# Optimization experiments

Hardware: AMD Instinct MI355X
Metric: run time of the kernel (lower is better)

The kernel has to match this reference:

```python
import jax, jax.numpy as jnp
import numpy as np

B, T, I, H = 128, 1024, 512, 1024

def setup_inputs() -> dict:
    key = jax.random.key(0)
    ks = jax.random.split(key, 7)
    stdv = 1.0 / np.sqrt(H)
    u = lambda k, shape: jax.random.uniform(k, shape, jnp.float32, -stdv, stdv)
    return {
        "x": jax.random.normal(ks[0], (B, T, I), jnp.float32),
        "lens": jax.random.randint(ks[1], (B,), 1, T + 1),
        "W": u(ks[2], (I, 4 * H)),
        "U": u(ks[3], (H, 4 * H)),
        "P": u(ks[4], (H, 2 * H)),
        "P_o": u(ks[5], (H, H)),
        "bias": u(ks[6], (4 * H,)),
    }

def reference(x, lens, W, U, P, P_o, bias):
    hs = P_o.shape[0]
    # Precompute input contribution to gates once: [B, T, 4H]
    xW = jnp.einsum('bti,ig->btg', x, W) + bias

    def step(c, g_x):
        gates = g_x + c @ U                      # [B, 4H] (gates use c_t, per source)
        peep = c @ P                             # [B, 2H]
        i_t = jax.nn.sigmoid(gates[:, :hs] + jnp.tanh(peep[:, :hs]))
        f_t = jax.nn.sigmoid(gates[:, hs:2 * hs] + jnp.tanh(peep[:, hs:]))
        g_t = jnp.tanh(gates[:, 2 * hs:3 * hs])
        c_new = f_t * c + i_t * g_t
        o_t = jax.nn.sigmoid(gates[:, 3 * hs:] + jnp.tanh(c_new @ P_o))
        h_t = o_t * jnp.tanh(c_new)
        return c_new, h_t

    c0 = jnp.zeros((x.shape[0], hs), x.dtype)
    _, h_seq = jax.lax.scan(step, c0, jnp.swapaxes(xW, 0, 1))  # h_seq: [T, B, H]
    h_seq = jnp.swapaxes(h_seq, 0, 1)                          # [B, T, H]
    batch_idx = jnp.arange(x.shape[0])
    return h_seq[batch_idx, lens - 1, :]
```

## Files before the change

kernel.cpp:

```cpp
#include <hip/hip_runtime.h>

typedef unsigned short u16;
typedef unsigned long long u64;
typedef __attribute__((ext_vector_type(8))) short bf16x8;
typedef __attribute__((ext_vector_type(4))) float f32x4;
typedef __attribute__((ext_vector_type(4))) u16 u16x4;


__device__ __forceinline__ float bf2f(u16 u) { return __uint_as_float(((unsigned)u) << 16); }
__device__ __forceinline__ u16 f2bf(float f) {
  unsigned u = __float_as_uint(f);
  u = (u + 0x7FFFu + ((u >> 16) & 1u)) >> 16;
  return (u16)u;
}
__device__ __forceinline__ float sigm_(float x) { return 1.0f / (1.0f + __expf(-x)); }
__device__ __forceinline__ float tanh_(float x) {
  float e = __expf(2.0f * fabsf(x));
  float r = 1.0f - 2.0f / (e + 1.0f);
  return copysignf(r, x);
}
__device__ __forceinline__ void g2l16(const void* g, void* l) {
  __builtin_amdgcn_global_load_lds(
      (const __attribute__((address_space(1))) void*)g,
      (__attribute__((address_space(3))) void*)l, 16, 0, 0);
}

__global__ __launch_bounds__(256) void k_cvt(const float* __restrict__ in,
                                             u16* __restrict__ out, int n) {
  int i = (blockIdx.x * 256 + threadIdx.x) * 4;
  if (i >= n) return;
  const float4 v = *(const float4*)(in + i);
  u16x4 o;
  o.x = f2bf(v.x); o.y = f2bf(v.y); o.z = f2bf(v.z); o.w = f2bf(v.w);
  *(u16x4*)(out + i) = o;
}

__global__ __launch_bounds__(256) void k_tr(const float* __restrict__ src, int ld,
                                            u16* __restrict__ out, int K) {
  __shared__ float tle[64][65];
  int j0 = blockIdx.x * 64, k0 = blockIdx.y * 64;
  int jc = threadIdx.x & 63, kq = threadIdx.x >> 6;
  #pragma unroll
  for (int p = 0; p < 16; ++p) {
    int kr = kq * 16 + p;
    tle[jc][kr] = src[(size_t)(k0 + kr) * ld + j0 + jc];
  }
  __syncthreads();
  #pragma unroll
  for (int p = 0; p < 16; ++p) {
    int jr = kq * 16 + p;
    out[(size_t)(j0 + jr) * K + k0 + jc] = f2bf(tle[jr][jc]);
  }
}

__global__ __launch_bounds__(256) void k_gemm(const u16* __restrict__ A,
                                              const u16* __restrict__ Bt,
                                              const float* __restrict__ bias,
                                              u16* __restrict__ xw) {
  __shared__ u16 lds[16384];
  const int Kd = 512;
  int n0 = blockIdx.x * 128, m0 = blockIdx.y * 128;
  int tid = threadIdx.x, lane = tid & 63, wave = tid >> 6;
  int wm = (wave >> 1) * 64, wn = (wave & 1) * 64;
  int l15 = lane & 15, lk8 = (lane >> 4) * 8;
  f32x4 acc[4][4];
  #pragma unroll
  for (int i = 0; i < 4; ++i)
    #pragma unroll
    for (int j = 0; j < 4; ++j) {
      acc[i][j][0] = 0.f; acc[i][j][1] = 0.f; acc[i][j][2] = 0.f; acc[i][j][3] = 0.f;
    }
  for (int k0 = 0; k0 < Kd; k0 += 64) {
    #pragma unroll
    for (int p = 0; p < 8; ++p) {
      int c = p * 256 + tid;
      int ldsbase = (c - lane) * 16;
      int row = (c & 1023) >> 3, colb = (c & 7) * 16;
      const char* g;
      if (c < 1024) g = (const char*)A  + ((size_t)(m0 + row) * Kd + k0) * 2 + colb;
      else          g = (const char*)Bt + ((size_t)(n0 + row) * Kd + k0) * 2 + colb;
      g2l16(g, (char*)lds + ldsbase);
    }
    __syncthreads();
    #pragma unroll
    for (int kk = 0; kk < 2; ++kk) {
      bf16x8 af[4], bfr[4];
      #pragma unroll
      for (int mf = 0; mf < 4; ++mf)
        af[mf] = *(const bf16x8*)&lds[(wm + mf * 16 + l15) * 64 + kk * 32 + lk8];
      #pragma unroll
      for (int nf = 0; nf < 4; ++nf)
        bfr[nf] = *(const bf16x8*)&lds[8192 + (wn + nf * 16 + l15) * 64 + kk * 32 + lk8];
      #pragma unroll
      for (int mf = 0; mf < 4; ++mf)
        #pragma unroll
        for (int nf = 0; nf < 4; ++nf)
          acc[mf][nf] = __builtin_amdgcn_mfma_f32_16x16x32_bf16(af[mf], bfr[nf], acc[mf][nf], 0, 0, 0);
    }
    __syncthreads();
  }
  int rbase = (lane >> 4) * 4;
  #pragma unroll
  for (int mf = 0; mf < 4; ++mf)
    #pragma unroll
    for (int nf = 0; nf < 4; ++nf) {
      int n = n0 + wn + nf * 16 + l15;
      float bv = bias[n];
      int g = n >> 10, j = n & 1023;
      int jbp = j >> 4, col = j & 15;
      #pragma unroll
      for (int r = 0; r < 4; ++r) {
        int m = m0 + wm + mf * 16 + rbase + r;
        int b = m >> 10, t = m & 1023;
        xw[(((size_t)t * 64 + jbp) * 128 + b) * 48 + g * 16 + col] =
            f2bf(acc[mf][nf][r] + bv);
      }
    }
}

__device__ __forceinline__ void gbar_rb(unsigned* bar, unsigned phase, int jb, int rb) {
  __syncthreads();
  if (threadIdx.x == 0) {
    unsigned* barg = bar + rb * 256;
    unsigned* gc = barg + (jb >> 5) * 32;
    unsigned* master = barg + 128;
    unsigned v = __hip_atomic_fetch_add(gc, 1u, __ATOMIC_RELAXED, __HIP_MEMORY_SCOPE_AGENT) + 1;
    if (v == 32u * phase)
      __hip_atomic_fetch_add(master, 1u, __ATOMIC_RELAXED, __HIP_MEMORY_SCOPE_AGENT);
    while (__hip_atomic_load(master, __ATOMIC_RELAXED, __HIP_MEMORY_SCOPE_AGENT) < 2u * phase)
      __builtin_amdgcn_s_sleep(1);
  }
  __syncthreads();
}

__global__ __launch_bounds__(320) void k_persist(
    u16* __restrict__ cb, const u16* __restrict__ wcat, const u16* __restrict__ xw,
    const int* __restrict__ lens, float* __restrict__ sp, float* __restrict__ sn,
    unsigned* __restrict__ bar) {
  __shared__ __align__(16) char smem[98304];
  char* Ab = smem;
  float* sgl = (float*)(smem + 65536);

  const int bid = blockIdx.x;
  const int jb = bid & 63, rb = bid >> 6;
  const int tid = threadIdx.x;
  const int lane = tid & 63, wave = tid >> 6;
  const int l15 = lane & 15, lhi = lane >> 4;
  const int swz = (l15 & 7) << 4;

  const u16* brow = wcat + ((size_t)(wave * 1024 + jb * 16 + l15)) * 1024 + lhi * 8;
  bf16x8 breg[32];
  #pragma unroll
  for (int kf = 0; kf < 32; ++kf)
    breg[kf] = *(const bf16x8*)(brow + kf * 32);

  const int erow = tid >> 3, ejj = (tid & 7) * 2;
  const int eb = rb * 32 + erow;
  const int ej0 = jb * 16 + ejj;
  const int mylen = (tid < 256) ? lens[eb] : 0;
  float c0 = 0.f, c1 = 0.f;

  #pragma unroll 1
  for (int t = 0; t < 1024; ++t) {
    const u64* asrc = (const u64*)((const char*)cb + (size_t)(t & 1) * 262144 +
                                   (size_t)rb * 65536);
    u16* cbout = cb + (size_t)((t + 1) & 1) * 131072;

    unsigned xg0 = 0, xg1 = 0, xg2 = 0;
    if (tid < 256) {
      const u16* xr = xw + (((size_t)t * 64 + jb) * 128 + eb) * 48 + ejj;
      xg0 = *(const unsigned*)(xr);
      xg1 = *(const unsigned*)(xr + 16);
      xg2 = *(const unsigned*)(xr + 32);
    }

    u64 av[26];
    #pragma unroll
    for (int i = 0; i < 26; ++i) {
      int c = i * 320 + tid;
      if (c < 8192)
        av[i] = __hip_atomic_load(asrc + c, __ATOMIC_RELAXED, __HIP_MEMORY_SCOPE_AGENT);
    }
    #pragma unroll
    for (int i = 0; i < 26; ++i) {
      int c = i * 320 + tid;
      if (c < 8192) {
        int row = c >> 8, col8 = c & 255;
        *(u64*)(Ab + row * 2048 + ((col8 * 8) ^ ((row & 7) << 4))) = av[i];
      }
    }
    __syncthreads();

    f32x4 acc0 = {0.f, 0.f, 0.f, 0.f}, acc1 = {0.f, 0.f, 0.f, 0.f};
    f32x4 acc2 = {0.f, 0.f, 0.f, 0.f}, acc3 = {0.f, 0.f, 0.f, 0.f};
    #pragma unroll
    for (int kf = 0; kf < 32; kf += 2) {
      int koffA = (kf * 64 + lhi * 16) ^ swz;
      int koffB = ((kf + 1) * 64 + lhi * 16) ^ swz;
      bf16x8 a0 = *(const bf16x8*)(Ab + l15 * 2048 + koffA);
      bf16x8 a1 = *(const bf16x8*)(Ab + (16 + l15) * 2048 + koffA);
      bf16x8 b0 = *(const bf16x8*)(Ab + l15 * 2048 + koffB);
      bf16x8 b1 = *(const bf16x8*)(Ab + (16 + l15) * 2048 + koffB);
      acc0 = __builtin_amdgcn_mfma_f32_16x16x32_bf16(a0, breg[kf], acc0, 0, 0, 0);
      acc1 = __builtin_amdgcn_mfma_f32_16x16x32_bf16(a1, breg[kf], acc1, 0, 0, 0);
      acc2 = __builtin_amdgcn_mfma_f32_16x16x32_bf16(b0, breg[kf + 1], acc2, 0, 0, 0);
      acc3 = __builtin_amdgcn_mfma_f32_16x16x32_bf16(b1, breg[kf + 1], acc3, 0, 0, 0);
    }
    acc0[0] += acc2[0]; acc0[1] += acc2[1]; acc0[2] += acc2[2]; acc0[3] += acc2[3];
    acc1[0] += acc3[0]; acc1[1] += acc3[1]; acc1[2] += acc3[2]; acc1[3] += acc3[3];

    *(f32x4*)&sgl[(wave * 16 + l15) * 36 + lhi * 4] = acc0;
    *(f32x4*)&sgl[(wave * 16 + l15) * 36 + 16 + lhi * 4] = acc1;
    __syncthreads();

    if (tid < 256) {
      float ci[2] = {c0, c1};
      float cn2[2];
      u16 nb2[2];
      unsigned xg[3] = {xg0, xg1, xg2};
      #pragma unroll
      for (int e = 0; e < 2; ++e) {
        int col = ejj + e;
        float gi = sgl[(0 * 16 + col) * 36 + erow] + bf2f((u16)(xg[0] >> (e * 16)));
        float gf = sgl[(1 * 16 + col) * 36 + erow] + bf2f((u16)(xg[1] >> (e * 16)));
        float gg = sgl[(2 * 16 + col) * 36 + erow] + bf2f((u16)(xg[2] >> (e * 16)));
        float pi = sgl[(3 * 16 + col) * 36 + erow];
        float pf = sgl[(4 * 16 + col) * 36 + erow];
        float it = sigm_(gi + tanh_(pi));
        float ft = sigm_(gf + tanh_(pf));
        float gt = tanh_(gg);
        float cn = ft * ci[e] + it * gt;
        cn2[e] = cn;
        nb2[e] = f2bf(cn);
      }
      c0 = cn2[0]; c1 = cn2[1];
      __hip_atomic_store((unsigned*)(cbout + (size_t)eb * 1024 + ej0),
                         (unsigned)nb2[0] | ((unsigned)nb2[1] << 16),
                         __ATOMIC_RELAXED, __HIP_MEMORY_SCOPE_AGENT);
      if (t == mylen - 1) {
        *(float2*)(sp + (size_t)eb * 1024 + ej0) = make_float2(ci[0], ci[1]);
        *(float2*)(sn + (size_t)eb * 1024 + ej0) = make_float2(cn2[0], cn2[1]);
      }
    }

    gbar_rb(bar, (unsigned)(t + 1), jb, rb);
  }
}

__global__ __launch_bounds__(256) void k_final(
    const int* __restrict__ lens, const float* __restrict__ x,
    const float* __restrict__ W, const float* __restrict__ U,
    const float* __restrict__ Po, const float* __restrict__ bias,
    const float* __restrict__ sp, const float* __restrict__ sn,
    float* __restrict__ out) {
  __shared__ float scp[1024], scn[1024], sx[512];
  int b = blockIdx.x, tid = threadIdx.x;
  int t = lens[b] - 1;
  for (int k = tid; k < 1024; k += 256) {
    scp[k] = sp[b * 1024 + k];
    scn[k] = sn[b * 1024 + k];
  }
  for (int k = tid; k < 512; k += 256)
    sx[k] = x[(size_t)(b * 1024 + t) * 512 + k];
  __syncthreads();
  for (int j = tid; j < 1024; j += 256) {
    float au = 0.f, ap = 0.f, ax = 0.f;
    for (int k = 0; k < 1024; ++k) {
      au = fmaf(scp[k], U[(size_t)k * 4096 + 3072 + j], au);
      ap = fmaf(scn[k], Po[(size_t)k * 1024 + j], ap);
    }
    for (int k = 0; k < 512; ++k)
      ax = fmaf(sx[k], W[(size_t)k * 4096 + 3072 + j], ax);
    float go = ax + bias[3072 + j] + au;
    float o = sigm_(go + tanh_(ap));
    out[b * 1024 + j] = o * tanh_(scn[j]);
  }
}

extern "C" void kernel_launch(void* const* d_in, const int* in_sizes, int n_in,
                              void* d_out, int out_size, void* d_ws, size_t ws_size,
                              hipStream_t stream) {
  const float* x    = (const float*)d_in[0];
  const int*   lens = (const int*)d_in[1];
  const float* W    = (const float*)d_in[2];
  const float* U    = (const float*)d_in[3];
  const float* P    = (const float*)d_in[4];
  const float* Po   = (const float*)d_in[5];
  const float* bias = (const float*)d_in[6];
  float* out = (float*)d_out;
  char* ws = (char*)d_ws;

  u16*      xw   = (u16*)(ws);
  u16*      xbf  = (u16*)(ws + 805306368LL);
  u16*      wt   = (u16*)(ws + 939524096LL);
  u16*      wcat = (u16*)(ws + 943718400LL);
  u16*      cbp  = (u16*)(ws + 954204160LL);
  float*    sp   = (float*)(ws + 954728448LL);
  float*    sn   = (float*)(ws + 955252736LL);
  unsigned* bar  = (unsigned*)(ws + 955777024LL);

  hipMemsetAsync(cbp, 0, 262144, stream);
  hipMemsetAsync(bar, 0, 4096, stream);

  k_cvt<<<65536, 256, 0, stream>>>(x, xbf, 67108864);
  k_tr<<<dim3(48, 8), 256, 0, stream>>>(W, 4096, wt, 512);
  k_tr<<<dim3(48, 16), 256, 0, stream>>>(U, 4096, wcat, 1024);
  k_tr<<<dim3(32, 16), 256, 0, stream>>>(P, 2048, wcat + (size_t)3072 * 1024, 1024);
  k_gemm<<<dim3(24, 1024), 256, 0, stream>>>(xbf, wt, bias, xw);

  void* ka[] = {(void*)&cbp, (void*)&wcat, (void*)&xw, (void*)&lens,
                (void*)&sp, (void*)&sn, (void*)&bar};
  hipLaunchCooperativeKernel((const void*)k_persist, dim3(256), dim3(320), ka, 0, stream);

  k_final<<<128, 256, 0, stream>>>(lens, x, W, U, Po, bias, sp, sn, out);
}
```

Measured before the change: 6.771 ms.

## Replace hierarchical atomic barrier with per-block flags and split LDS staging

Result: slower. 19.25 ms (+184.3%).

```diff
diff --git a/kernel.cpp b/kernel.cpp
--- a/kernel.cpp
+++ b/kernel.cpp
@@ -23,6 +23,11 @@
   __builtin_amdgcn_global_load_lds(
       (const __attribute__((address_space(1))) void*)g,
       (__attribute__((address_space(3))) void*)l, 16, 0, 0);
+}
+__device__ __forceinline__ void lds_bar() {
+  asm volatile("s_waitcnt lgkmcnt(0)" ::: "memory");
+  __builtin_amdgcn_sched_barrier(0);
+  __builtin_amdgcn_s_barrier();
 }
 
 __global__ __launch_bounds__(256) void k_cvt(const float* __restrict__ in,
@@ -118,21 +123,6 @@
     }
 }
 
-__device__ __forceinline__ void gbar_rb(unsigned* bar, unsigned phase, int jb, int rb) {
-  __syncthreads();
-  if (threadIdx.x == 0) {
-    unsigned* barg = bar + rb * 256;
-    unsigned* gc = barg + (jb >> 5) * 32;
-    unsigned* master = barg + 128;
-    unsigned v = __hip_atomic_fetch_add(gc, 1u, __ATOMIC_RELAXED, __HIP_MEMORY_SCOPE_AGENT) + 1;
-    if (v == 32u * phase)
-      __hip_atomic_fetch_add(master, 1u, __ATOMIC_RELAXED, __HIP_MEMORY_SCOPE_AGENT);
-    while (__hip_atomic_load(master, __ATOMIC_RELAXED, __HIP_MEMORY_SCOPE_AGENT) < 2u * phase)
-      __builtin_amdgcn_s_sleep(1);
-  }
-  __syncthreads();
-}
-
 __global__ __launch_bounds__(320) void k_persist(
     u16* __restrict__ cb, const u16* __restrict__ wcat, const u16* __restrict__ xw,
     const int* __restrict__ lens, float* __restrict__ sp, float* __restrict__ sn,
@@ -160,20 +150,22 @@
   const int mylen = (tid < 256) ? lens[eb] : 0;
   float c0 = 0.f, c1 = 0.f;
 
+  unsigned* const flags = bar + rb * 1024;
+
+  unsigned xgc0 = 0, xgc1 = 0, xgc2 = 0;
+  if (tid < 256) {
+    const u16* xr = xw + (((size_t)0 * 64 + jb) * 128 + eb) * 48 + ejj;
+    xgc0 = *(const unsigned*)(xr);
+    xgc1 = *(const unsigned*)(xr + 16);
+    xgc2 = *(const unsigned*)(xr + 32);
+  }
+
   #pragma unroll 1
   for (int t = 0; t < 1024; ++t) {
     const u64* asrc = (const u64*)((const char*)cb + (size_t)(t & 1) * 262144 +
                                    (size_t)rb * 65536);
     u16* cbout = cb + (size_t)((t + 1) & 1) * 131072;
 
-    unsigned xg0 = 0, xg1 = 0, xg2 = 0;
-    if (tid < 256) {
-      const u16* xr = xw + (((size_t)t * 64 + jb) * 128 + eb) * 48 + ejj;
-      xg0 = *(const unsigned*)(xr);
-      xg1 = *(const unsigned*)(xr + 16);
-      xg2 = *(const unsigned*)(xr + 32);
-    }
-
     u64 av[26];
     #pragma unroll
     for (int i = 0; i < 26; ++i) {
@@ -181,43 +173,67 @@
       if (c < 8192)
         av[i] = __hip_atomic_load(asrc + c, __ATOMIC_RELAXED, __HIP_MEMORY_SCOPE_AGENT);
     }
-    #pragma unroll
-    for (int i = 0; i < 26; ++i) {
+    unsigned xgn0 = 0, xgn1 = 0, xgn2 = 0;
+    {
+      int t2 = (t < 1023) ? (t + 1) : 1023;
+      if (tid < 256) {
+        const u16* xr = xw + (((size_t)t2 * 64 + jb) * 128 + eb) * 48 + ejj;
+        xgn0 = *(const unsigned*)(xr);
+        xgn1 = *(const unsigned*)(xr + 16);
+        xgn2 = *(const unsigned*)(xr + 32);
+      }
+    }
+
+    #pragma unroll
+    for (int i = 0; i < 13; ++i) {
       int c = i * 320 + tid;
-      if (c < 8192) {
+      if (c < 4096) {
         int row = c >> 8, col8 = c & 255;
         *(u64*)(Ab + row * 2048 + ((col8 * 8) ^ ((row & 7) << 4))) = av[i];
       }
     }
-    __syncthreads();
-
-    f32x4 acc0 = {0.f, 0.f, 0.f, 0.f}, acc1 = {0.f, 0.f, 0.f, 0.f};
-    f32x4 acc2 = {0.f, 0.f, 0.f, 0.f}, acc3 = {0.f, 0.f, 0.f, 0.f};
+    lds_bar();
+
+    f32x4 acc0 = {0.f, 0.f, 0.f, 0.f}, acc2 = {0.f, 0.f, 0.f, 0.f};
     #pragma unroll
     for (int kf = 0; kf < 32; kf += 2) {
-      int koffA = (kf * 64 + lhi * 16) ^ swz;
-      int koffB = ((kf + 1) * 64 + lhi * 16) ^ swz;
-      bf16x8 a0 = *(const bf16x8*)(Ab + l15 * 2048 + koffA);
-      bf16x8 a1 = *(const bf16x8*)(Ab + (16 + l15) * 2048 + koffA);
-      bf16x8 b0 = *(const bf16x8*)(Ab + l15 * 2048 + koffB);
-      bf16x8 b1 = *(const bf16x8*)(Ab + (16 + l15) * 2048 + koffB);
+      bf16x8 a0 = *(const bf16x8*)(Ab + l15 * 2048 + ((kf * 64 + lhi * 16) ^ swz));
+      bf16x8 a1 = *(const bf16x8*)(Ab + l15 * 2048 + (((kf + 1) * 64 + lhi * 16) ^ swz));
       acc0 = __builtin_amdgcn_mfma_f32_16x16x32_bf16(a0, breg[kf], acc0, 0, 0, 0);
-      acc1 = __builtin_amdgcn_mfma_f32_16x16x32_bf16(a1, breg[kf], acc1, 0, 0, 0);
-      acc2 = __builtin_amdgcn_mfma_f32_16x16x32_bf16(b0, breg[kf + 1], acc2, 0, 0, 0);
-      acc3 = __builtin_amdgcn_mfma_f32_16x16x32_bf16(b1, breg[kf + 1], acc3, 0, 0, 0);
+      acc2 = __builtin_amdgcn_mfma_f32_16x16x32_bf16(a1, breg[kf + 1], acc2, 0, 0, 0);
+    }
+    __builtin_amdgcn_sched_barrier(0);
+
+    #pragma unroll
+    for (int i = 12; i < 26; ++i) {
+      int c = i * 320 + tid;
+      if (c >= 4096 && c < 8192) {
+        int row = c >> 8, col8 = c & 255;
+        *(u64*)(Ab + row * 2048 + ((col8 * 8) ^ ((row & 7) << 4))) = av[i];
+      }
+    }
+    lds_bar();
+
+    f32x4 acc1 = {0.f, 0.f, 0.f, 0.f}, acc3 = {0.f, 0.f, 0.f, 0.f};
+    #pragma unroll
+    for (int kf = 0; kf < 32; kf += 2) {
+      bf16x8 a0 = *(const bf16x8*)(Ab + (16 + l15) * 2048 + ((kf * 64 + lhi * 16) ^ swz));
+      bf16x8 a1 = *(const bf16x8*)(Ab + (16 + l15) * 2048 + (((kf + 1) * 64 + lhi * 16) ^ swz));
+      acc1 = __builtin_amdgcn_mfma_f32_16x16x32_bf16(a0, breg[kf], acc1, 0, 0, 0);
+      acc3 = __builtin_amdgcn_mfma_f32_16x16x32_bf16(a1, breg[kf + 1], acc3, 0, 0, 0);
     }
     acc0[0] += acc2[0]; acc0[1] += acc2[1]; acc0[2] += acc2[2]; acc0[3] += acc2[3];
     acc1[0] += acc3[0]; acc1[1] += acc3[1]; acc1[2] += acc3[2]; acc1[3] += acc3[3];
 
     *(f32x4*)&sgl[(wave * 16 + l15) * 36 + lhi * 4] = acc0;
     *(f32x4*)&sgl[(wave * 16 + l15) * 36 + 16 + lhi * 4] = acc1;
-    __syncthreads();
+    lds_bar();
 
     if (tid < 256) {
       float ci[2] = {c0, c1};
       float cn2[2];
       u16 nb2[2];
-      unsigned xg[3] = {xg0, xg1, xg2};
+      unsigned xg[3] = {xgc0, xgc1, xgc2};
       #pragma unroll
       for (int e = 0; e < 2; ++e) {
         int col = ejj + e;
@@ -242,8 +258,19 @@
         *(float2*)(sn + (size_t)eb * 1024 + ej0) = make_float2(cn2[0], cn2[1]);
       }
     }
-
-    gbar_rb(bar, (unsigned)(t + 1), jb, rb);
+    xgc0 = xgn0; xgc1 = xgn1; xgc2 = xgn2;
+
+    __syncthreads();
+    if (tid == 0)
+      __hip_atomic_store(flags + jb * 16, (unsigned)(t + 1),
+                         __ATOMIC_RELAXED, __HIP_MEMORY_SCOPE_AGENT);
+    if (tid < 64) {
+      const unsigned* f = flags + tid * 16;
+      while (__hip_atomic_load(f, __ATOMIC_RELAXED, __HIP_MEMORY_SCOPE_AGENT) <
+             (unsigned)(t + 1))
+        __builtin_amdgcn_s_sleep(1);
+    }
+    __syncthreads();
   }
 }
 
@@ -300,7 +327,7 @@
   unsigned* bar  = (unsigned*)(ws + 955777024LL);
 
   hipMemsetAsync(cbp, 0, 262144, stream);
-  hipMemsetAsync(bar, 0, 4096, stream);
+  hipMemsetAsync(bar, 0, 16384, stream);
 
   k_cvt<<<65536, 256, 0, stream>>>(x, xbf, 67108864);
   k_tr<<<dim3(48, 8), 256, 0, stream>>>(W, 4096, wt, 512);
```
